# Kernel optimization log

Measured on AMD Instinct MI355X. Metric: run time of the kernel, lower is better.

## Reference

```python
import jax, jax.numpy as jnp
import numpy as np

# Module hyperparameters (from init_kwargs / submodule semantics)
B, N, C, H = 32, 1024, 192, 3
D = C // H                      # head_dim = 64
TAU_MIN = 0.1                   # LearnableTemperature: tau = tau_min + softplus(p)
P_MAX = 0.3                     # LearnedHeadDropout: rate = p_max * sigmoid(logit)
ANNEAL_START = 2.0              # TemperatureScheduler: mult = start -> 1 over training
TRAIN_PROGRESS = 0.5            # scalar forward arg (fixed)


def setup_inputs() -> dict:
    key = jax.random.key(0)
    ks = jax.random.split(key, 8)
    x = jax.random.normal(ks[0], (B, N, C), jnp.float32)
    qkv_w = jax.random.normal(ks[1], (3 * C, C), jnp.float32) * 0.02
    qkv_b = jnp.zeros((3 * C,), jnp.float32)
    proj_w = jax.random.normal(ks[2], (C, C), jnp.float32) * 0.02
    proj_b = jnp.zeros((C,), jnp.float32)
    temp_param = jax.random.normal(ks[3], (H,), jnp.float32) * 0.1
    dropout_logits = jax.random.normal(ks[4], (H,), jnp.float32) * 0.1
    residual_param = jnp.zeros((), jnp.float32)
    tau_aleatoric = jax.random.uniform(ks[5], (B, H), jnp.float32) * 0.5
    return {"x": x, "qkv_w": qkv_w, "qkv_b": qkv_b, "proj_w": proj_w,
            "proj_b": proj_b, "temp_param": temp_param,
            "dropout_logits": dropout_logits, "residual_param": residual_param,
            "tau_aleatoric": tau_aleatoric}


def reference(x, qkv_w, qkv_b, proj_w, proj_b, temp_param, dropout_logits,
              residual_param, tau_aleatoric):
    b, n, c = x.shape
    scale = D ** -0.5
    # QKV projection -> (3, B, H, N, D)
    qkv = (x @ qkv_w.T + qkv_b).reshape(b, n, 3, H, D).transpose(2, 0, 3, 1, 4)
    q, k, v = qkv[0], qkv[1], qkv[2]
    # epistemic per-head temperature with curriculum annealing
    tau_e = TAU_MIN + jax.nn.softplus(temp_param)            # (H,)
    anneal = ANNEAL_START - (ANNEAL_START - 1.0) * TRAIN_PROGRESS
    tau_e = tau_e * anneal
    # combine with aleatoric temperature: (B, H, 1, 1)
    tau = tau_aleatoric[:, :, None, None] + tau_e[None, :, None, None]
    # attention scores with per-head temperature scaling
    attn = jnp.einsum('bhnd,bhmd->bhnm', q, k) * scale / tau  # (B,H,N,N)
    attn = jax.nn.softmax(attn, axis=-1)
    # early-exit confidence: mean over heads and queries of max attn prob
    confidence = attn.max(axis=-1).mean(axis=(1, 2))          # (B,)
    # learned head dropout (deterministic eval form: scale by keep prob)
    keep = 1.0 - P_MAX * jax.nn.sigmoid(dropout_logits)       # (H,)
    attn_d = attn * keep[None, :, None, None]
    # attention output + projection
    out = jnp.einsum('bhnm,bhmd->bnhd', attn_d, v).reshape(b, n, c)
    out = out @ proj_w.T + proj_b
    # learned residual blend
    w = jax.nn.sigmoid(residual_param)
    out = w * out + (1.0 - w) * x
    return out, confidence
```

## Files before the change

### kernel.cpp

```cpp
#include <hip/hip_runtime.h>

#define BB 32
#define NN 1024
#define CC 192
#define HH 3
#define DD 64
#define BHND 6291456

typedef __bf16 bf16x8 __attribute__((ext_vector_type(8)));
typedef float  f32x4  __attribute__((ext_vector_type(4)));

__device__ __align__(16) unsigned short g_q  [BHND];
__device__ __align__(16) unsigned short g_k  [BHND];
__device__ __align__(16) unsigned short g_vt [BHND];
__device__ __align__(16) unsigned short g_ao [BHND];
__device__ __align__(16) unsigned short g_wb [3 * CC * CC];
__device__ __align__(16) unsigned short g_pwb[CC * CC];
__device__ float g_conf[BB];

__device__ __forceinline__ unsigned short f2b(float f) {
    union { float f; unsigned int i; } z; z.f = f;
    return (unsigned short)((z.i + 0x7fffu + ((z.i >> 16) & 1u)) >> 16);
}

__global__ __launch_bounds__(256) void convert_kernel(
    const float* __restrict__ qw, const float* __restrict__ pw)
{
    const int u = blockIdx.x * 256 + threadIdx.x;
    if (blockIdx.x == 0 && threadIdx.x < BB) g_conf[threadIdx.x] = 0.0f;
    const float* src; unsigned short* dstb; int p;
    if (u < 27648) { src = qw; dstb = g_wb;  p = u; }
    else           { src = pw; dstb = g_pwb; p = u - 27648; }
    const int jh   = p & 1;
    const int lane = (p >> 1) & 63;
    const int fg   = p >> 7;
    const int kh   = fg % 6;
    const int t    = fg / 6;
    const int mq   = lane & 15;
    const int q    = lane >> 4;
    const int col  = t * 16 + mq;
    const int k    = kh * 32 + q * 8 + jh * 4;
    const float4 v = *(const float4*)(src + (size_t)col * CC + k);
    const unsigned int a = (unsigned int)f2b(v.x) | ((unsigned int)f2b(v.y) << 16);
    const unsigned int b = (unsigned int)f2b(v.z) | ((unsigned int)f2b(v.w) << 16);
    *(uint2*)(dstb + (size_t)p * 4) = make_uint2(a, b);
}

__global__ __launch_bounds__(256, 4) void qkv_kernel(
    const float* __restrict__ x,
    const float* __restrict__ bias,
    const float* __restrict__ tp,
    const float* __restrict__ ta)
{
    const int tid   = threadIdx.x;
    const int wv    = tid >> 6;
    const int lane  = tid & 63;
    const int q     = lane >> 4;
    const int mq    = lane & 15;
    const int strip = wv >> 1;
    const int half  = wv & 1;
    const int base  = blockIdx.x * 32;
    const int b     = base >> 10;
    const int nloc  = (base & 1023) + strip * 16;

    __shared__ __align__(16) unsigned short xa[32 * 200];
    const float* xb = x + (size_t)base * CC;
    #pragma unroll
    for (int c = 0; c < 6; ++c) {
        const int f   = c * 256 + tid;
        const float4 u = *(const float4*)(xb + (size_t)f * 4);
        const int row = f / 48;
        const int kk  = (f - row * 48) * 4;
        const unsigned int a  = (unsigned int)f2b(u.x) | ((unsigned int)f2b(u.y) << 16);
        const unsigned int b2 = (unsigned int)f2b(u.z) | ((unsigned int)f2b(u.w) << 16);
        *(uint2*)(&xa[row * 200 + kk]) = make_uint2(a, b2);
    }
    __syncthreads();

    bf16x8 af[6];
    #pragma unroll
    for (int kh = 0; kh < 6; ++kh)
        af[kh] = *(const bf16x8*)(&xa[(strip * 16 + mq) * 200 + kh * 32 + q * 8]);

    float mult_h[HH];
    if (half == 0) {
        #pragma unroll
        for (int h = 0; h < HH; ++h) {
            const float tau_e = (0.1f + logf(1.0f + __expf(tp[h]))) * 1.5f;
            mult_h[h] = (0.125f * 1.4426950408889634f) / (ta[b * 3 + h] + tau_e);
        }
    } else {
        mult_h[0] = mult_h[1] = mult_h[2] = 1.0f;
    }

    const int tbase = half * 12;
    unsigned short* const dst = half ? g_k : g_q;
    bf16x8 bcur[6];
    #pragma unroll
    for (int kh = 0; kh < 6; ++kh)
        bcur[kh] = *(const bf16x8*)(g_wb + ((size_t)(tbase * 6 + kh) * 64 + lane) * 8);
    #pragma unroll 2
    for (int ot = 0; ot < 12; ++ot) {
        bf16x8 bnxt[6];
        if (ot < 11) {
            #pragma unroll
            for (int kh = 0; kh < 6; ++kh)
                bnxt[kh] = *(const bf16x8*)(g_wb + ((size_t)((tbase + ot + 1) * 6 + kh) * 64 + lane) * 8);
        }
        f32x4 acc = (f32x4){0.f,0.f,0.f,0.f};
        #pragma unroll
        for (int kh = 0; kh < 6; ++kh)
            acc = __builtin_amdgcn_mfma_f32_16x16x32_bf16(af[kh], bcur[kh], acc, 0, 0, 0);
        const int col = ot * 16;
        const float bv = bias[half * 192 + col + mq];
        const int h = col >> 6, d0 = col & 63;
        const float m = mult_h[h];
        unsigned short* dp = dst + ((size_t)((b * 3 + h) * NN + nloc + q * 4)) * DD + d0 + mq;
        #pragma unroll
        for (int r = 0; r < 4; ++r)
            dp[(size_t)r * DD] = f2b((acc[r] + bv) * m);
        #pragma unroll
        for (int kh = 0; kh < 6; ++kh) bcur[kh] = bnxt[kh];
    }

    const int vbase = 24 + half * 6;
    #pragma unroll
    for (int kh = 0; kh < 6; ++kh)
        bcur[kh] = *(const bf16x8*)(g_wb + ((size_t)(vbase * 6 + kh) * 64 + lane) * 8);
    #pragma unroll 2
    for (int ot = 0; ot < 6; ++ot) {
        const int dd0 = half * 96 + ot * 16;
        bf16x8 bnxt[6];
        if (ot < 5) {
            #pragma unroll
            for (int kh = 0; kh < 6; ++kh)
                bnxt[kh] = *(const bf16x8*)(g_wb + ((size_t)((vbase + ot + 1) * 6 + kh) * 64 + lane) * 8);
        }
        f32x4 acc = (f32x4){0.f,0.f,0.f,0.f};
        #pragma unroll
        for (int kh = 0; kh < 6; ++kh)
            acc = __builtin_amdgcn_mfma_f32_16x16x32_bf16(bcur[kh], af[kh], acc, 0, 0, 0);
        #pragma unroll
        for (int r = 0; r < 4; ++r) {
            const int dd = dd0 + q * 4 + r;
            const int h = dd >> 6, d = dd & 63;
            const float bv = bias[384 + dd];
            g_vt[((size_t)((b * 3 + h) * DD + d)) * NN + nloc + mq] = f2b(acc[r] + bv);
        }
        #pragma unroll
        for (int kh = 0; kh < 6; ++kh) bcur[kh] = bnxt[kh];
    }
}

__global__ __launch_bounds__(256, 3) void attn_kernel(
    const float* __restrict__ dl)
{
    const int tid  = threadIdx.x;
    const int wv   = tid >> 6;
    const int lane = tid & 63;
    const int q    = lane >> 4;
    const int mq   = lane & 15;

    const int xcd = blockIdx.x & 7;
    const int ii  = blockIdx.x >> 3;
    const int bh  = xcd * 12 + (ii >> 3);
    const int n0  = (ii & 7) * 128;
    const int b  = bh / 3;
    const int h  = bh - b * 3;
    const float keep = 1.0f - 0.3f / (1.0f + __expf(-dl[h]));

    __shared__ __align__(16) unsigned short ks[2][4096];
    __shared__ __align__(16) unsigned short vt[2][4096];
    __shared__ __align__(16) unsigned short pt[8192];
    __shared__ float conf_s[128];

    const size_t qra = (size_t)(bh * NN + n0 + wv * 16 + mq) * DD;
    const size_t qrb = qra + (size_t)64 * DD;
    const bf16x8 qfa0 = *(const bf16x8*)(g_q + qra + q * 8);
    const bf16x8 qfa1 = *(const bf16x8*)(g_q + qra + 32 + q * 8);
    const bf16x8 qfb0 = *(const bf16x8*)(g_q + qrb + q * 8);
    const bf16x8 qfb1 = *(const bf16x8*)(g_q + qrb + 32 + q * 8);

    const size_t krow0 = (size_t)(bh * NN + wv * 16 + mq) * DD;
    const size_t vrow  = (size_t)(bh * DD + wv * 16 + mq) * NN;
    bf16x8 kr0 = *(const bf16x8*)(g_k + krow0 + q * 8);
    bf16x8 kr1 = *(const bf16x8*)(g_k + krow0 + 32 + q * 8);
    bf16x8 vr0 = *(const bf16x8*)(g_vt + vrow + q * 8);
    bf16x8 vr1 = *(const bf16x8*)(g_vt + vrow + 32 + q * 8);

    f32x4 oa[4], ob[4];
    #pragma unroll
    for (int i = 0; i < 4; ++i) { oa[i] = (f32x4){0.f,0.f,0.f,0.f}; ob[i] = (f32x4){0.f,0.f,0.f,0.f}; }
    float la = 0.0f, lb = 0.0f, pma = 0.0f, pmb = 0.0f;

    for (int it = 0; it < 16; ++it) {
        const int cur = it & 1;
        ((bf16x8*)ks[cur])[tid]       = kr0;
        ((bf16x8*)ks[cur])[256 + tid] = kr1;
        ((bf16x8*)vt[cur])[tid]       = vr0;
        ((bf16x8*)vt[cur])[256 + tid] = vr1;
        __syncthreads();

        if (it < 15) {
            const int t1 = (it + 1) * 64;
            kr0 = *(const bf16x8*)(g_k + krow0 + (size_t)t1 * DD + q * 8);
            kr1 = *(const bf16x8*)(g_k + krow0 + (size_t)t1 * DD + 32 + q * 8);
            vr0 = *(const bf16x8*)(g_vt + vrow + t1 + q * 8);
            vr1 = *(const bf16x8*)(g_vt + vrow + t1 + 32 + q * 8);
        }

        f32x4 sa[4], sb[4];
        #pragma unroll
        for (int i = 0; i < 4; ++i) { sa[i] = (f32x4){0.f,0.f,0.f,0.f}; sb[i] = (f32x4){0.f,0.f,0.f,0.f}; }
        __builtin_amdgcn_s_setprio(1);
        #pragma unroll
        for (int kh = 0; kh < 2; ++kh) {
            const bf16x8 qfa = kh ? qfa1 : qfa0;
            const bf16x8 qfb = kh ? qfb1 : qfb0;
            #pragma unroll
            for (int kt = 0; kt < 4; ++kt) {
                const bf16x8 afr = ((const bf16x8*)ks[cur])[kh * 256 + kt * 64 + lane];
                sa[kt] = __builtin_amdgcn_mfma_f32_16x16x32_bf16(afr, qfa, sa[kt], 0, 0, 0);
                sb[kt] = __builtin_amdgcn_mfma_f32_16x16x32_bf16(afr, qfb, sb[kt], 0, 0, 0);
            }
        }
        __builtin_amdgcn_s_setprio(0);

        #pragma unroll
        for (int s = 0; s < 2; ++s) {
            unsigned short* ptb = pt + s * 4096;
            #pragma unroll
            for (int kt = 0; kt < 4; ++kt) {
                const f32x4 sv = s ? sb[kt] : sa[kt];
                const float p0 = __builtin_amdgcn_exp2f(sv[0]);
                const float p1 = __builtin_amdgcn_exp2f(sv[1]);
                const float p2 = __builtin_amdgcn_exp2f(sv[2]);
                const float p3 = __builtin_amdgcn_exp2f(sv[3]);
                const float mx = fmaxf(fmaxf(p0, p1), fmaxf(p2, p3));
                if (s) { pmb = fmaxf(pmb, mx); lb += (p0 + p1) + (p2 + p3); }
                else   { pma = fmaxf(pma, mx); la += (p0 + p1) + (p2 + p3); }
                const unsigned int ua = __builtin_amdgcn_perm(
                    __float_as_uint(p1), __float_as_uint(p0), 0x07060302u);
                const unsigned int ub = __builtin_amdgcn_perm(
                    __float_as_uint(p3), __float_as_uint(p2), 0x07060302u);
                const int kh2   = kt >> 1;
                const int qk    = (kt * 2 + (q >> 1)) & 3;
                const int chunk = ((wv * 2 + kh2) * 4 + qk) * 16 + mq;
                *(uint2*)((char*)ptb + chunk * 16 + (q & 1) * 8) = make_uint2(ua, ub);
            }
        }
        __builtin_amdgcn_s_waitcnt(0xC07F);

        __builtin_amdgcn_s_setprio(1);
        #pragma unroll
        for (int kh = 0; kh < 2; ++kh) {
            const bf16x8 pfa = ((const bf16x8*)pt)[(wv * 2 + kh) * 64 + lane];
            const bf16x8 pfb = ((const bf16x8*)(pt + 4096))[(wv * 2 + kh) * 64 + lane];
            #pragma unroll
            for (int ctv = 0; ctv < 4; ++ctv) {
                const bf16x8 vf = ((const bf16x8*)vt[cur])[kh * 256 + ctv * 64 + lane];
                oa[ctv] = __builtin_amdgcn_mfma_f32_16x16x32_bf16(pfa, vf, oa[ctv], 0, 0, 0);
                ob[ctv] = __builtin_amdgcn_mfma_f32_16x16x32_bf16(pfb, vf, ob[ctv], 0, 0, 0);
            }
        }
        __builtin_amdgcn_s_setprio(0);
    }

    float l0 = la, l1 = lb;
    l0 += __shfl_xor(l0, 16, 64); l0 += __shfl_xor(l0, 32, 64);
    l1 += __shfl_xor(l1, 16, 64); l1 += __shfl_xor(l1, 32, 64);
    float p0 = pma, p1 = pmb;
    p0 = fmaxf(p0, __shfl_xor(p0, 16, 64)); p0 = fmaxf(p0, __shfl_xor(p0, 32, 64));
    p1 = fmaxf(p1, __shfl_xor(p1, 16, 64)); p1 = fmaxf(p1, __shfl_xor(p1, 32, 64));
    const float invla = 1.0f / l0;
    const float invlb = 1.0f / l1;

    if (lane < 16) {
        conf_s[wv * 16 + mq]      = p0 * invla;
        conf_s[64 + wv * 16 + mq] = p1 * invlb;
    }
    __syncthreads();
    if (tid < 64) {
        float v = conf_s[tid] + conf_s[64 + tid];
        #pragma unroll
        for (int off = 1; off <= 32; off <<= 1) v += __shfl_xor(v, off, 64);
        if (tid == 0) atomicAdd(&g_conf[b], v);
    }

    #pragma unroll
    for (int s = 0; s < 2; ++s) {
        const float invl = s ? invlb : invla;
        float sc[4];
        #pragma unroll
        for (int r = 0; r < 4; ++r)
            sc[r] = keep * __int_as_float(
                __builtin_amdgcn_ds_bpermute((q * 4 + r) << 2, __float_as_int(invl)));
        #pragma unroll
        for (int ctv = 0; ctv < 4; ++ctv)
            #pragma unroll
            for (int r = 0; r < 4; ++r) {
                const f32x4 o = s ? ob[ctv] : oa[ctv];
                g_ao[((size_t)(b * NN + n0 + s * 64 + wv * 16 + q * 4 + r)) * CC + h * DD + ctv * 16 + mq] =
                    f2b(o[r] * sc[r]);
            }
    }
}

__global__ __launch_bounds__(256, 4) void proj_kernel(
    const float* __restrict__ pb,
    const float* __restrict__ rp,
    const float* __restrict__ x,
    float* __restrict__ out,
    float* __restrict__ out_c)
{
    const int tid   = threadIdx.x;
    const int wv    = tid >> 6;
    const int lane  = tid & 63;
    const int q     = lane >> 4;
    const int mq    = lane & 15;
    const int strip = wv >> 1;
    const int half  = wv & 1;
    const int base  = blockIdx.x * 32;
    const int r0    = base + strip * 16;

    if (blockIdx.x == 0 && tid < BB)
        out_c[tid] = g_conf[tid] * (1.0f / (float)(HH * NN));

    const float wres = 1.0f / (1.0f + __expf(-rp[0]));

    __shared__ __align__(16) unsigned short xa[32 * 200];
    const unsigned short* aob = g_ao + (size_t)base * CC;
    #pragma unroll
    for (int c = 0; c < 3; ++c) {
        const int f   = c * 256 + tid;
        const int row = f / 24;
        const int k8  = (f - row * 24) * 8;
        *(bf16x8*)(&xa[row * 200 + k8]) = *(const bf16x8*)(aob + (size_t)f * 8);
    }
    __syncthreads();

    bf16x8 af[6];
    #pragma unroll
    for (int kh = 0; kh < 6; ++kh)
        af[kh] = *(const bf16x8*)(&xa[(strip * 16 + mq) * 200 + kh * 32 + q * 8]);

    const int tbase = half * 6;
    bf16x8 bcur[6];
    #pragma unroll
    for (int kh = 0; kh < 6; ++kh)
        bcur[kh] = *(const bf16x8*)(g_pwb + ((size_t)(tbase * 6 + kh) * 64 + lane) * 8);
    #pragma unroll 2
    for (int ot = 0; ot < 6; ++ot) {
        const int o0 = half * 96 + ot * 16;
        bf16x8 bnxt[6];
        if (ot < 5) {
            #pragma unroll
            for (int kh = 0; kh < 6; ++kh)
                bnxt[kh] = *(const bf16x8*)(g_pwb + ((size_t)((tbase + ot + 1) * 6 + kh) * 64 + lane) * 8);
        }
        f32x4 acc = (f32x4){0.f,0.f,0.f,0.f};
        #pragma unroll
        for (int kh = 0; kh < 6; ++kh)
            acc = __builtin_amdgcn_mfma_f32_16x16x32_bf16(af[kh], bcur[kh], acc, 0, 0, 0);
        const float bv = pb[o0 + mq];
        #pragma unroll
        for (int r = 0; r < 4; ++r) {
            const int n = r0 + q * 4 + r;
            const float xv = x[(size_t)n * CC + o0 + mq];
            out[(size_t)n * CC + o0 + mq] = wres * (acc[r] + bv) + (1.0f - wres) * xv;
        }
        #pragma unroll
        for (int kh = 0; kh < 6; ++kh) bcur[kh] = bnxt[kh];
    }
}

extern "C" void kernel_launch(void* const* d_in, const int* in_sizes, int n_in,
                              void* d_out, int out_size, void* d_ws, size_t ws_size,
                              hipStream_t stream)
{
    const float* x  = (const float*)d_in[0];
    const float* qw = (const float*)d_in[1];
    const float* qb = (const float*)d_in[2];
    const float* pw = (const float*)d_in[3];
    const float* pb = (const float*)d_in[4];
    const float* tp = (const float*)d_in[5];
    const float* dl = (const float*)d_in[6];
    const float* rp = (const float*)d_in[7];
    const float* ta = (const float*)d_in[8];

    float* out   = (float*)d_out;
    float* out_c = out + (size_t)BB * NN * CC;

    convert_kernel<<<144, 256, 0, stream>>>(qw, pw);
    qkv_kernel<<<(BB * NN) / 32, 256, 0, stream>>>(x, qb, tp, ta);
    attn_kernel<<<BB * HH * (NN / 128), 256, 0, stream>>>(dl);
    proj_kernel<<<(BB * NN) / 32, 256, 0, stream>>>(pb, rp, x, out, out_c);
}
```

Before: 160.7 us.

## Pre-pack K/V into MFMA fragment layout and read fragments directly from global

The QKV projection now writes K and V into a tiled layout that matches the MFMA operand fragments, per 64-key tile. The attention kernel loads these fragments straight from global memory. This removes the LDS double buffers for K/V, the register staging and the per-iteration __syncthreads. The aim is to cut LDS traffic and barrier stalls, and to free LDS for occupancy. In exchange, every wave in a block now fetches the same K/V fragments separately through the cache, and those loads are no longer prefetched one tile ahead, so global-load latency may be exposed.

```diff
diff --git a/kernel.cpp b/kernel.cpp
--- a/kernel.cpp
+++ b/kernel.cpp
@@ -11,8 +11,8 @@
 typedef float  f32x4  __attribute__((ext_vector_type(4)));
 
 __device__ __align__(16) unsigned short g_q  [BHND];
-__device__ __align__(16) unsigned short g_k  [BHND];
-__device__ __align__(16) unsigned short g_vt [BHND];
+__device__ __align__(16) unsigned short g_kp [BHND];
+__device__ __align__(16) unsigned short g_vp [BHND];
 __device__ __align__(16) unsigned short g_ao [BHND];
 __device__ __align__(16) unsigned short g_wb [3 * CC * CC];
 __device__ __align__(16) unsigned short g_pwb[CC * CC];
@@ -93,8 +93,12 @@
         mult_h[0] = mult_h[1] = mult_h[2] = 1.0f;
     }
 
+    const int t_  = nloc >> 6;
+    const int kt_ = (nloc >> 4) & 3;
+    const int khv = (nloc >> 5) & 1;
+    const int hiv = ((nloc >> 3) + (mq >> 3)) & 3;
+
     const int tbase = half * 12;
-    unsigned short* const dst = half ? g_k : g_q;
     bf16x8 bcur[6];
     #pragma unroll
     for (int kh = 0; kh < 6; ++kh)
@@ -114,11 +118,20 @@
         const int col = ot * 16;
         const float bv = bias[half * 192 + col + mq];
         const int h = col >> 6, d0 = col & 63;
-        const float m = mult_h[h];
-        unsigned short* dp = dst + ((size_t)((b * 3 + h) * NN + nloc + q * 4)) * DD + d0 + mq;
-        #pragma unroll
-        for (int r = 0; r < 4; ++r)
-            dp[(size_t)r * DD] = f2b((acc[r] + bv) * m);
+        if (half == 0) {
+            const float m = mult_h[h];
+            unsigned short* dp = g_q + ((size_t)((b * 3 + h) * NN + nloc + q * 4)) * DD + d0 + mq;
+            #pragma unroll
+            for (int r = 0; r < 4; ++r)
+                dp[(size_t)r * DD] = f2b((acc[r] + bv) * m);
+        } else {
+            const int kh_ = d0 >> 5;
+            const int hi  = ((d0 >> 3) + (mq >> 3)) & 3;
+            unsigned short* cp = g_kp + ((size_t)(((b * 3 + h) * 16 + t_) * 8 + kh_ * 4 + kt_)) * 512;
+            #pragma unroll
+            for (int r = 0; r < 4; ++r)
+                cp[(hi * 16 + q * 4 + r) * 8 + (mq & 7)] = f2b(acc[r] + bv);
+        }
         #pragma unroll
         for (int kh = 0; kh < 6; ++kh) bcur[kh] = bnxt[kh];
     }
@@ -143,9 +156,10 @@
         #pragma unroll
         for (int r = 0; r < 4; ++r) {
             const int dd = dd0 + q * 4 + r;
-            const int h = dd >> 6, d = dd & 63;
+            const int h = dd >> 6, dc = dd & 63, ctv = dc >> 4;
             const float bv = bias[384 + dd];
-            g_vt[((size_t)((b * 3 + h) * DD + d)) * NN + nloc + mq] = f2b(acc[r] + bv);
+            g_vp[((size_t)(((b * 3 + h) * 16 + t_) * 8 + khv * 4 + ctv)) * 512
+                 + (hiv * 16 + (dd & 15)) * 8 + (mq & 7)] = f2b(acc[r] + bv);
         }
         #pragma unroll
         for (int kh = 0; kh < 6; ++kh) bcur[kh] = bnxt[kh];
@@ -169,8 +183,6 @@
     const int h  = bh - b * 3;
     const float keep = 1.0f - 0.3f / (1.0f + __expf(-dl[h]));
 
-    __shared__ __align__(16) unsigned short ks[2][4096];
-    __shared__ __align__(16) unsigned short vt[2][4096];
     __shared__ __align__(16) unsigned short pt[8192];
     __shared__ float conf_s[128];
 
@@ -181,33 +193,13 @@
     const bf16x8 qfb0 = *(const bf16x8*)(g_q + qrb + q * 8);
     const bf16x8 qfb1 = *(const bf16x8*)(g_q + qrb + 32 + q * 8);
 
-    const size_t krow0 = (size_t)(bh * NN + wv * 16 + mq) * DD;
-    const size_t vrow  = (size_t)(bh * DD + wv * 16 + mq) * NN;
-    bf16x8 kr0 = *(const bf16x8*)(g_k + krow0 + q * 8);
-    bf16x8 kr1 = *(const bf16x8*)(g_k + krow0 + 32 + q * 8);
-    bf16x8 vr0 = *(const bf16x8*)(g_vt + vrow + q * 8);
-    bf16x8 vr1 = *(const bf16x8*)(g_vt + vrow + 32 + q * 8);
-
     f32x4 oa[4], ob[4];
     #pragma unroll
     for (int i = 0; i < 4; ++i) { oa[i] = (f32x4){0.f,0.f,0.f,0.f}; ob[i] = (f32x4){0.f,0.f,0.f,0.f}; }
     float la = 0.0f, lb = 0.0f, pma = 0.0f, pmb = 0.0f;
 
-    for (int it = 0; it < 16; ++it) {
-        const int cur = it & 1;
-        ((bf16x8*)ks[cur])[tid]       = kr0;
-        ((bf16x8*)ks[cur])[256 + tid] = kr1;
-        ((bf16x8*)vt[cur])[tid]       = vr0;
-        ((bf16x8*)vt[cur])[256 + tid] = vr1;
-        __syncthreads();
-
-        if (it < 15) {
-            const int t1 = (it + 1) * 64;
-            kr0 = *(const bf16x8*)(g_k + krow0 + (size_t)t1 * DD + q * 8);
-            kr1 = *(const bf16x8*)(g_k + krow0 + (size_t)t1 * DD + 32 + q * 8);
-            vr0 = *(const bf16x8*)(g_vt + vrow + t1 + q * 8);
-            vr1 = *(const bf16x8*)(g_vt + vrow + t1 + 32 + q * 8);
-        }
+    for (int t = 0; t < 16; ++t) {
+        const size_t cb = (size_t)(bh * 16 + t) * 4096;
 
         f32x4 sa[4], sb[4];
         #pragma unroll
@@ -219,7 +211,7 @@
             const bf16x8 qfb = kh ? qfb1 : qfb0;
             #pragma unroll
             for (int kt = 0; kt < 4; ++kt) {
-                const bf16x8 afr = ((const bf16x8*)ks[cur])[kh * 256 + kt * 64 + lane];
+                const bf16x8 afr = *(const bf16x8*)(g_kp + cb + (size_t)(kh * 4 + kt) * 512 + lane * 8);
                 sa[kt] = __builtin_amdgcn_mfma_f32_16x16x32_bf16(afr, qfa, sa[kt], 0, 0, 0);
                 sb[kt] = __builtin_amdgcn_mfma_f32_16x16x32_bf16(afr, qfb, sb[kt], 0, 0, 0);
             }
@@ -258,7 +250,7 @@
             const bf16x8 pfb = ((const bf16x8*)(pt + 4096))[(wv * 2 + kh) * 64 + lane];
             #pragma unroll
             for (int ctv = 0; ctv < 4; ++ctv) {
-                const bf16x8 vf = ((const bf16x8*)vt[cur])[kh * 256 + ctv * 64 + lane];
+                const bf16x8 vf = *(const bf16x8*)(g_vp + cb + (size_t)(kh * 4 + ctv) * 512 + lane * 8);
                 oa[ctv] = __builtin_amdgcn_mfma_f32_16x16x32_bf16(pfa, vf, oa[ctv], 0, 0, 0);
                 ob[ctv] = __builtin_amdgcn_mfma_f32_16x16x32_bf16(pfb, vf, ob[ctv], 0, 0, 0);
             }
```

New measurement: 181.9 us. 1.13x slower.
